# Kernel optimization log

Measured on AMD Instinct MI355X. Metric: run time of the kernel, lower is better.

Reference implementation:

```python
import jax, jax.numpy as jnp
import numpy as np

B, T, C, H = 2, 2048, 1024, 16
DH = C // H


def setup_inputs() -> dict:
    key = jax.random.key(0)
    ks = jax.random.split(key, 5)
    x = jax.random.normal(ks[0], (B, T, C), dtype=jnp.float32)
    qkv_w = jax.random.normal(ks[1], (3 * C, C), dtype=jnp.float32) * (C ** -0.5)
    qkv_b = jnp.zeros((3 * C,), dtype=jnp.float32)
    proj_w = jax.random.normal(ks[2], (C, C), dtype=jnp.float32) * (C ** -0.5)
    proj_b = jnp.zeros((C,), dtype=jnp.float32)
    # init_raw = log(exp(init_decay) - 1) with init_decay = 0.1
    init_raw = float(np.log(np.exp(0.1) - 1.0))
    lambda_raw = jnp.full((H,), init_raw, dtype=jnp.float32)
    return {"x": x, "qkv_w": qkv_w, "qkv_b": qkv_b,
            "proj_w": proj_w, "proj_b": proj_b, "lambda_raw": lambda_raw}


def reference(x, qkv_w, qkv_b, proj_w, proj_b, lambda_raw) -> jnp.ndarray:
    scale = DH ** -0.5
    # qkv projection: [B,T,3C] -> [3,B,H,T,DH]
    qkv = (jnp.einsum('btc,oc->bto', x, qkv_w) + qkv_b)
    qkv = qkv.reshape(B, T, 3, H, DH).transpose(2, 0, 3, 1, 4)
    q, k, v = qkv[0], qkv[1], qkv[2]
    # scores [B,H,T,T]
    attn = jnp.einsum('bhid,bhjd->bhij', q, k) * scale
    # learned per-head exponential decay mask (multiplicative, pre-softmax)
    lambdas = jax.nn.softplus(lambda_raw)  # [H]
    pos = jnp.arange(T, dtype=jnp.float32)
    dist = jnp.abs(pos[:, None] - pos[None, :])  # [T,T]
    decay = jnp.exp(-lambdas[None, :, None, None] * dist[None, None])  # [1,H,T,T]
    attn = jax.nn.softmax(attn * decay, axis=-1)
    out = jnp.einsum('bhij,bhjd->bhid', attn, v)  # [B,H,T,DH]
    out = out.transpose(0, 2, 1, 3).reshape(B, T, C)
    return jnp.einsum('btc,oc->bto', out, proj_w) + proj_b
```

## Files before the change

kernel.cpp:

```cpp
#include <hip/hip_runtime.h>
#include <cstdint>
#include <cstddef>


#define DEVI __device__ __forceinline__

typedef float f32x4 __attribute__((ext_vector_type(4)));
typedef short bf16x8 __attribute__((ext_vector_type(8)));

static constexpr int Bc = 2, Tc = 2048, Cc = 1024, Hc = 16, DHc = 64;

DEVI unsigned short f2bf(float f) {
  union { float f; unsigned u; } a; a.f = f;
  unsigned u = a.u;
  unsigned r = (u + 0x7fffu + ((u >> 16) & 1u)) >> 16;
  return (unsigned short)r;
}

DEVI float bf2f(unsigned short u) {
  union { unsigned u; float f; } a; a.u = ((unsigned)u) << 16;
  return a.f;
}

DEVI unsigned packbf(float lo, float hi) {
  return (unsigned)f2bf(lo) | ((unsigned)f2bf(hi) << 16);
}

DEVI void gload_lds16(const void* g, void* l) {
  __builtin_amdgcn_global_load_lds(
      (const __attribute__((address_space(1))) void*)g,
      (__attribute__((address_space(3))) void*)l, 16, 0, 0);
}

__global__ __launch_bounds__(256) void k_cvt(const float* __restrict__ in,
                                             unsigned short* __restrict__ out,
                                             int n4) {
  int i = blockIdx.x * 256 + threadIdx.x;
  if (i >= n4) return;
  const float4 v = ((const float4*)in)[i];
  ushort4 o;
  o.x = f2bf(v.x); o.y = f2bf(v.y); o.z = f2bf(v.z); o.w = f2bf(v.w);
  ((ushort4*)out)[i] = o;
}

template <int OUT_BF16>
__global__ __launch_bounds__(256) void k_gemm_nt(
    const unsigned short* __restrict__ A, const unsigned short* __restrict__ B,
    const float* __restrict__ bias, void* __restrict__ C, int K, int ldc) {
  __shared__ __align__(16) unsigned short As[128 * 32];
  __shared__ __align__(16) unsigned short Bs[128 * 32];
  const int tid = threadIdx.x, lane = tid & 63, wid = tid >> 6;
  const int wm = wid >> 1, wn = wid & 1;
  const int l15 = lane & 15, l4 = lane >> 4;
  f32x4 acc[4][4] = {};
  const int boff0 = wid * 2048 + lane * 16;
  for (int k0 = 0; k0 < K; k0 += 32) {
    __syncthreads();
#pragma unroll
    for (int s = 0; s < 2; ++s) {
      const int boff = boff0 + s * 1024;
      const int row = boff >> 6, colb = boff & 63;
      gload_lds16((const char*)A + ((size_t)(blockIdx.y * 128 + row) * K + k0) * 2 + colb,
                  (char*)As + (wid * 2 + s) * 1024);
      gload_lds16((const char*)B + ((size_t)(blockIdx.x * 128 + row) * K + k0) * 2 + colb,
                  (char*)Bs + (wid * 2 + s) * 1024);
    }
    __syncthreads();
    bf16x8 af[4], bf[4];
#pragma unroll
    for (int i = 0; i < 4; ++i) {
      af[i] = *(const bf16x8*)(As + (wm * 64 + i * 16 + l15) * 32 + l4 * 8);
      bf[i] = *(const bf16x8*)(Bs + (wn * 64 + i * 16 + l15) * 32 + l4 * 8);
    }
#pragma unroll
    for (int mi = 0; mi < 4; ++mi)
#pragma unroll
      for (int ni = 0; ni < 4; ++ni)
        acc[mi][ni] = __builtin_amdgcn_mfma_f32_16x16x32_bf16(af[mi], bf[ni],
                                                              acc[mi][ni], 0, 0, 0);
  }
#pragma unroll
  for (int mi = 0; mi < 4; ++mi) {
    const int r0 = blockIdx.y * 128 + wm * 64 + mi * 16 + l4 * 4;
#pragma unroll
    for (int ni = 0; ni < 4; ++ni) {
      const int c = blockIdx.x * 128 + wn * 64 + ni * 16 + l15;
      const float bv = bias[c];
#pragma unroll
      for (int j = 0; j < 4; ++j) {
        const float v = acc[mi][ni][j] + bv;
        if (OUT_BF16)
          ((unsigned short*)C)[(size_t)(r0 + j) * ldc + c] = f2bf(v);
        else
          ((float*)C)[(size_t)(r0 + j) * ldc + c] = v;
      }
    }
  }
}

__global__ __launch_bounds__(256) void k_vtrans(const unsigned short* __restrict__ qkv,
                                                unsigned short* __restrict__ vt,
                                                float* __restrict__ vsum) {
  __shared__ unsigned short tile[64][65];
  __shared__ float psum[4][64];
  const int bh = blockIdx.y, b = bh >> 4, h = bh & 15;
  const int t0 = blockIdx.x * 64;
  const int tid = threadIdx.x;
#pragma unroll
  for (int r = 0; r < 16; ++r) {
    const int e = r * 256 + tid;
    const int row = e >> 6, col = e & 63;
    tile[row][col] = qkv[(size_t)(b * Tc + t0 + row) * (3 * Cc) + 2 * Cc + h * DHc + col];
  }
  __syncthreads();
#pragma unroll
  for (int r = 0; r < 16; ++r) {
    const int e = r * 256 + tid;
    const int dd = e >> 6, tcol = e & 63;
    vt[((size_t)bh * DHc + dd) * Tc + t0 + tcol] = tile[tcol][dd];
  }
  const int d = tid & 63, part = tid >> 6;
  float s = 0.f;
#pragma unroll
  for (int k = 0; k < 16; ++k) s += bf2f(tile[part * 16 + k][d]);
  psum[part][d] = s;
  __syncthreads();
  if (tid < 64)
    vsum[((size_t)bh * 32 + blockIdx.x) * 64 + tid] =
        psum[0][tid] + psum[1][tid] + psum[2][tid] + psum[3][tid];
}

__global__ __launch_bounds__(64) void k_prefix(const float* __restrict__ vsum,
                                               float* __restrict__ vpre) {
  const int bh = blockIdx.x, d = threadIdx.x;
  float run = 0.f;
  for (int t = 0; t < 32; ++t) {
    vpre[((size_t)bh * 33 + t) * 64 + d] = run;
    run += vsum[((size_t)bh * 32 + t) * 64 + d];
  }
  vpre[((size_t)bh * 33 + 32) * 64 + d] = run;
}

__global__ __launch_bounds__(256, 2) void k_attn(const unsigned short* __restrict__ qkv,
                                                 const unsigned short* __restrict__ vt,
                                                 const float* __restrict__ lraw,
                                                 const float* __restrict__ vpre,
                                                 unsigned short* __restrict__ ao) {
  __shared__ __align__(16) unsigned short Ks[2][4096];
  __shared__ __align__(16) unsigned short Vs[2][4096];
  const int tid = threadIdx.x, lane = tid & 63, wid = tid >> 6;
  const int l15 = lane & 15, l4 = lane >> 4;
  const int bid = blockIdx.x;
  const int xcd = bid & 7, jj = bid >> 3;
  const int bh = xcd + 8 * (jj >> 4);
  const int qblk = jj & 15;
  const int b = bh >> 4, h = bh & 15;
  const float lam = log1pf(__expf(lraw[h]));
  const int qt0 = qblk * 8 + wid * 2;
  const int qA = qt0 * 16 + l15, qB = qA + 16;

  const int Dstar = (int)fminf(2048.0f, ceilf(18.5f / lam));
  const int q0 = qblk * 128;
  const int t_lo = (q0 > Dstar) ? ((q0 - Dstar) >> 6) : 0;
  const int t_end = min(32, (q0 + Dstar + 191) >> 6);
  const int nfar = 64 * t_lo + (Tc - 64 * t_end);

  const unsigned short* qpA = qkv + (size_t)(b * Tc + qA) * (3 * Cc) + h * DHc + l4 * 8;
  const unsigned short* qpB = qkv + (size_t)(b * Tc + qB) * (3 * Cc) + h * DHc + l4 * 8;
  const bf16x8 qfA0 = *(const bf16x8*)qpA, qfA1 = *(const bf16x8*)(qpA + 32);
  const bf16x8 qfB0 = *(const bf16x8*)qpB, qfB1 = *(const bf16x8*)(qpB + 32);

  const unsigned short* kSrc[2];
  const unsigned short* vSrc[2];
#pragma unroll
  for (int rr = 0; rr < 2; ++rr) {
    const int slot = (rr * 4 + wid) * 64 + lane;
    const int row = slot >> 3, wu = slot & 7;
    kSrc[rr] = qkv + (size_t)(b * Tc + row) * (3 * Cc) + Cc + h * DHc + 8 * (wu ^ (row & 7));
    vSrc[rr] = vt + (size_t)(bh * DHc + row) * Tc + 8 * (wu ^ (row & 7));
  }
  constexpr size_t KTS = (size_t)64 * 3 * Cc;
  int koffs[2][4], voffs[2][4];
#pragma unroll
  for (int hf = 0; hf < 2; ++hf) {
    const int r0 = hf * 32 + l15, r1 = r0 + 16;
    koffs[hf][0] = r0 * 128 + ((l4 ^ (r0 & 7)) * 16);
    koffs[hf][1] = r0 * 128 + (((4 + l4) ^ (r0 & 7)) * 16);
    koffs[hf][2] = r1 * 128 + ((l4 ^ (r1 & 7)) * 16);
    koffs[hf][3] = r1 * 128 + (((4 + l4) ^ (r1 & 7)) * 16);
#pragma unroll
    for (int db = 0; db < 4; ++db) {
      const int rv = db * 16 + l15;
      voffs[hf][db] = rv * 128 + (((hf * 4 + l4) ^ (rv & 7)) * 16);
    }
  }

  const int src0 = l15 | ((l4 & 1) << 5);
  const bool hi = (l4 >= 2);

  f32x4 oA[4], oB[4];
  {
    const float* pre_lo = vpre + ((size_t)bh * 33 + t_lo) * 64;
    const float* pre_hi = vpre + ((size_t)bh * 33 + t_end) * 64;
    const float* pre_all = vpre + ((size_t)bh * 33 + 32) * 64;
#pragma unroll
    for (int di = 0; di < 4; ++di)
#pragma unroll
      for (int j = 0; j < 4; ++j) {
        const int d = di * 16 + l4 * 4 + j;
        const float far = pre_lo[d] + (pre_all[d] - pre_hi[d]);
        oA[di][j] = far;
        oB[di][j] = far;
      }
  }
  float lsumA = 0.f, lsumB = 0.f;

#define STAGE(bb, t)                                                          \
  do {                                                                        \
    _Pragma("unroll") for (int rr = 0; rr < 2; ++rr) {                        \
      gload_lds16(kSrc[rr] + (size_t)(t) * KTS, &Ks[bb][(rr * 4 + wid) * 512]); \
      gload_lds16(vSrc[rr] + (t) * 64, &Vs[bb][(rr * 4 + wid) * 512]);        \
    }                                                                         \
  } while (0)

#define QTILE_P(zz0, zz1, delta_, lsum_, pf_)                                 \
  do {                                                                        \
    float p0[4], p1[4];                                                       \
    _Pragma("unroll") for (int r = 0; r < 4; ++r) {                           \
      const float d0 = 0.125f * __expf(-lam * (float)abs((delta_) - r));      \
      const float d1 = 0.125f * __expf(-lam * (float)abs((delta_) - 16 - r)); \
      p0[r] = __expf(zz0[r] * d0);                                            \
      p1[r] = __expf(zz1[r] * d1);                                            \
      lsum_ += p0[r] + p1[r];                                                 \
    }                                                                         \
    const unsigned pk00 = packbf(p0[0], p0[1]);                               \
    const unsigned pk01 = packbf(p0[2], p0[3]);                               \
    const unsigned pk10 = packbf(p1[0], p1[1]);                               \
    const unsigned pk11 = packbf(p1[2], p1[3]);                               \
    const unsigned a0 = __shfl(pk00, src0, 64), b0 = __shfl(pk10, src0, 64);  \
    const unsigned a1 = __shfl(pk01, src0, 64), b1 = __shfl(pk11, src0, 64);  \
    const unsigned a2 = __shfl(pk00, src0 + 16, 64),                          \
                   b2 = __shfl(pk10, src0 + 16, 64);                          \
    const unsigned a3 = __shfl(pk01, src0 + 16, 64),                          \
                   b3 = __shfl(pk11, src0 + 16, 64);                          \
    pf_.u[0] = hi ? b0 : a0;                                                  \
    pf_.u[1] = hi ? b1 : a1;                                                  \
    pf_.u[2] = hi ? b2 : a2;                                                  \
    pf_.u[3] = hi ? b3 : a3;                                                  \
  } while (0)

#define COMPUTE(bb, kb0)                                                          \
  do {                                                                            \
    const char* kL = (const char*)&Ks[bb][0];                                     \
    const char* vL = (const char*)&Vs[bb][0];                                     \
    _Pragma("unroll") for (int hf = 0; hf < 2; ++hf) {                            \
      const bf16x8 kg0 = *(const bf16x8*)(kL + koffs[hf][0]);                     \
      const bf16x8 kg1 = *(const bf16x8*)(kL + koffs[hf][1]);                     \
      const bf16x8 kg2 = *(const bf16x8*)(kL + koffs[hf][2]);                     \
      const bf16x8 kg3 = *(const bf16x8*)(kL + koffs[hf][3]);                     \
      f32x4 zA0 = {}, zA1 = {}, zB0 = {}, zB1 = {};                               \
      __builtin_amdgcn_s_setprio(1);                                              \
      zA0 = __builtin_amdgcn_mfma_f32_16x16x32_bf16(kg0, qfA0, zA0, 0, 0, 0);     \
      zA0 = __builtin_amdgcn_mfma_f32_16x16x32_bf16(kg1, qfA1, zA0, 0, 0, 0);     \
      zA1 = __builtin_amdgcn_mfma_f32_16x16x32_bf16(kg2, qfA0, zA1, 0, 0, 0);     \
      zA1 = __builtin_amdgcn_mfma_f32_16x16x32_bf16(kg3, qfA1, zA1, 0, 0, 0);     \
      zB0 = __builtin_amdgcn_mfma_f32_16x16x32_bf16(kg0, qfB0, zB0, 0, 0, 0);     \
      zB0 = __builtin_amdgcn_mfma_f32_16x16x32_bf16(kg1, qfB1, zB0, 0, 0, 0);     \
      zB1 = __builtin_amdgcn_mfma_f32_16x16x32_bf16(kg2, qfB0, zB1, 0, 0, 0);     \
      zB1 = __builtin_amdgcn_mfma_f32_16x16x32_bf16(kg3, qfB1, zB1, 0, 0, 0);     \
      __builtin_amdgcn_s_setprio(0);                                              \
      const int dA = qA - (kb0) - hf * 32 - l4 * 4;                               \
      const int dB = dA + 16;                                                     \
      union { unsigned u[4]; bf16x8 v; } pfA, pfB;                                \
      QTILE_P(zA0, zA1, dA, lsumA, pfA);                                          \
      QTILE_P(zB0, zB1, dB, lsumB, pfB);                                          \
      const bf16x8 v0 = *(const bf16x8*)(vL + voffs[hf][0]);                      \
      const bf16x8 v1 = *(const bf16x8*)(vL + voffs[hf][1]);                      \
      const bf16x8 v2 = *(const bf16x8*)(vL + voffs[hf][2]);                      \
      const bf16x8 v3 = *(const bf16x8*)(vL + voffs[hf][3]);                      \
      __builtin_amdgcn_s_setprio(1);                                              \
      oA[0] = __builtin_amdgcn_mfma_f32_16x16x32_bf16(v0, pfA.v, oA[0], 0, 0, 0); \
      oA[1] = __builtin_amdgcn_mfma_f32_16x16x32_bf16(v1, pfA.v, oA[1], 0, 0, 0); \
      oA[2] = __builtin_amdgcn_mfma_f32_16x16x32_bf16(v2, pfA.v, oA[2], 0, 0, 0); \
      oA[3] = __builtin_amdgcn_mfma_f32_16x16x32_bf16(v3, pfA.v, oA[3], 0, 0, 0); \
      oB[0] = __builtin_amdgcn_mfma_f32_16x16x32_bf16(v0, pfB.v, oB[0], 0, 0, 0); \
      oB[1] = __builtin_amdgcn_mfma_f32_16x16x32_bf16(v1, pfB.v, oB[1], 0, 0, 0); \
      oB[2] = __builtin_amdgcn_mfma_f32_16x16x32_bf16(v2, pfB.v, oB[2], 0, 0, 0); \
      oB[3] = __builtin_amdgcn_mfma_f32_16x16x32_bf16(v3, pfB.v, oB[3], 0, 0, 0); \
      __builtin_amdgcn_s_setprio(0);                                              \
    }                                                                             \
  } while (0)

  STAGE(0, t_lo);
  __syncthreads();
  for (int t = t_lo; t < t_end; ++t) {
    const int bb = (t - t_lo) & 1;
    const int tn = (t + 1 < t_end) ? (t + 1) : t_lo;
    STAGE(bb ^ 1, tn);
    COMPUTE(bb, t * 64);
    __syncthreads();
  }
#undef STAGE
#undef QTILE_P
#undef COMPUTE

  lsumA += __shfl_xor(lsumA, 16, 64);
  lsumA += __shfl_xor(lsumA, 32, 64);
  lsumB += __shfl_xor(lsumB, 16, 64);
  lsumB += __shfl_xor(lsumB, 32, 64);
  const float rlA = __builtin_amdgcn_rcpf(lsumA + (float)nfar);
  const float rlB = __builtin_amdgcn_rcpf(lsumB + (float)nfar);

  unsigned short* aopA = ao + (size_t)(b * Tc + qA) * Cc + h * DHc + l4 * 4;
  unsigned short* aopB = ao + (size_t)(b * Tc + qB) * Cc + h * DHc + l4 * 4;
#pragma unroll
  for (int di = 0; di < 4; ++di)
#pragma unroll
    for (int j = 0; j < 4; ++j) {
      aopA[di * 16 + j] = f2bf(oA[di][j] * rlA);
      aopB[di * 16 + j] = f2bf(oB[di][j] * rlB);
    }
}

extern "C" void kernel_launch(void* const* d_in, const int* in_sizes, int n_in,
                              void* d_out, int out_size, void* d_ws, size_t ws_size,
                              hipStream_t stream) {
  const float* x      = (const float*)d_in[0];
  const float* qkv_w  = (const float*)d_in[1];
  const float* qkv_b  = (const float*)d_in[2];
  const float* proj_w = (const float*)d_in[3];
  const float* proj_b = (const float*)d_in[4];
  const float* lraw   = (const float*)d_in[5];

  unsigned short* xb    = (unsigned short*)d_ws;
  unsigned short* wqkv  = xb + 4194304;
  unsigned short* wproj = wqkv + 3145728;
  unsigned short* qkvo  = wproj + 1048576;
  unsigned short* vt    = qkvo + 12582912;
  float*          vsum  = (float*)(vt + 4194304);
  float*          vpre  = vsum + 65536;
  unsigned short* ao    = xb;

  k_cvt<<<4096, 256, 0, stream>>>(x, xb, 1048576);
  k_cvt<<<3072, 256, 0, stream>>>(qkv_w, wqkv, 786432);
  k_cvt<<<1024, 256, 0, stream>>>(proj_w, wproj, 262144);
  k_gemm_nt<1><<<dim3(24, 32), 256, 0, stream>>>(xb, wqkv, qkv_b, qkvo, 1024, 3072);
  k_vtrans<<<dim3(32, 32), 256, 0, stream>>>(qkvo, vt, vsum);
  k_prefix<<<32, 64, 0, stream>>>(vsum, vpre);
  k_attn<<<512, 256, 0, stream>>>(qkvo, vt, lraw, vpre, ao);
  k_gemm_nt<0><<<dim3(8, 32), 256, 0, stream>>>(ao, wproj, proj_b, d_out, 1024, 1024);
}
```

Measured before the change: 187.3 us.

## Replace QKV projection GEMM with 256x256 tiled, LDS-staged, pipelined MFMA kernel

Adds a new GEMM kernel for the QKV projection. It uses 256x256 block tiles with 8 waves, direct global-to-LDS loads with an XOR swizzle, and a double-buffered, phased prefetch schedule using explicit waitcnt, barriers and setprio. It also remaps block indices to improve L2 locality. The aim is more data reuse per tile and overlap of memory loads with MFMA compute. In exchange it uses more LDS and registers, and launches only 192 blocks, which may underfill the GPU.

```diff
diff --git a/kernel.cpp b/kernel.cpp
--- a/kernel.cpp
+++ b/kernel.cpp
@@ -89,6 +89,129 @@
 #pragma unroll
       for (int j = 0; j < 4; ++j) {
         const float v = acc[mi][ni][j] + bv;
+        if (OUT_BF16)
+          ((unsigned short*)C)[(size_t)(r0 + j) * ldc + c] = f2bf(v);
+        else
+          ((float*)C)[(size_t)(r0 + j) * ldc + c] = v;
+      }
+    }
+  }
+}
+
+template <int OUT_BF16>
+__global__ __launch_bounds__(512, 2) void k_gemm256(
+    const unsigned short* __restrict__ A, const unsigned short* __restrict__ B,
+    const float* __restrict__ bias, void* __restrict__ C,
+    int K, int ldc, int NB) {
+  __shared__ __align__(16) unsigned short AS[2][2][8192];
+  __shared__ __align__(16) unsigned short BS[2][2][8192];
+  const int tid = threadIdx.x, lane = tid & 63, wid = tid >> 6;
+  const int wm = wid >> 2, wn = wid & 3;
+  const int l15 = lane & 15, l4 = lane >> 4;
+  const int swz = (blockIdx.x & 7) * (gridDim.x >> 3) + (blockIdx.x >> 3);
+  const int blockM = (swz / NB) * 256, blockN = (swz % NB) * 256;
+
+  const unsigned short* aS[2];
+  const unsigned short* bS[2];
+  char* aD[2]; char* bD[2];
+#pragma unroll
+  for (int g = 0; g < 2; ++g) {
+    const int r = wid * 16 + g * 8 + (lane >> 3);
+    const int cu = ((lane & 7) ^ (r & 7)) * 8;
+    aS[g] = A + (size_t)(blockM + r) * K + cu;
+    bS[g] = B + (size_t)(blockN + r) * K + cu;
+    aD[g] = (char*)&AS[0][0][(wid * 2 + g) * 512];
+    bD[g] = (char*)&BS[0][0][(wid * 2 + g) * 512];
+  }
+  const int T = K >> 6;
+
+#define SG_A(d, h, t)                                                          \
+  do { _Pragma("unroll") for (int g = 0; g < 2; ++g)                           \
+    gload_lds16(aS[g] + (size_t)(h) * 128 * K + (t) * 64,                      \
+                aD[g] + ((d) * 2 + (h)) * 16384); } while (0)
+#define SG_B(d, h, t)                                                          \
+  do { _Pragma("unroll") for (int g = 0; g < 2; ++g)                           \
+    gload_lds16(bS[g] + (size_t)(h) * 128 * K + (t) * 64,                      \
+                bD[g] + ((d) * 2 + (h)) * 16384); } while (0)
+
+  int aoff[4][2], boff[2][2];
+#pragma unroll
+  for (int mt = 0; mt < 4; ++mt)
+#pragma unroll
+    for (int kh = 0; kh < 2; ++kh) {
+      const int r = wm * 64 + mt * 16 + l15;
+      aoff[mt][kh] = r * 128 + (((kh * 4 + l4) ^ (r & 7)) * 16);
+    }
+#pragma unroll
+  for (int nt = 0; nt < 2; ++nt)
+#pragma unroll
+    for (int kh = 0; kh < 2; ++kh) {
+      const int r = wn * 32 + nt * 16 + l15;
+      boff[nt][kh] = r * 128 + (((kh * 4 + l4) ^ (r & 7)) * 16);
+    }
+
+  f32x4 acc[8][4] = {};
+
+  SG_A(0, 0, 0); SG_B(0, 0, 0); SG_A(0, 1, 0); SG_B(0, 1, 0);
+  if (T > 1) {
+    SG_A(1, 0, 1); SG_B(1, 0, 1);
+    asm volatile("s_waitcnt vmcnt(4)" ::: "memory");
+  } else {
+    asm volatile("s_waitcnt vmcnt(0)" ::: "memory");
+  }
+  __builtin_amdgcn_s_barrier();
+  __builtin_amdgcn_sched_barrier(0);
+
+#define PHASE(d, qm, qn, STG, VMODE)                                           \
+  do {                                                                         \
+    const char* aL = (const char*)&AS[d][qm][0];                               \
+    const char* bL = (const char*)&BS[d][qn][0];                               \
+    bf16x8 af[4][2], bfr[2][2];                                                \
+    _Pragma("unroll") for (int mt = 0; mt < 4; ++mt)                           \
+      _Pragma("unroll") for (int kh = 0; kh < 2; ++kh)                         \
+        af[mt][kh] = *(const bf16x8*)(aL + aoff[mt][kh]);                      \
+    _Pragma("unroll") for (int nt = 0; nt < 2; ++nt)                           \
+      _Pragma("unroll") for (int kh = 0; kh < 2; ++kh)                         \
+        bfr[nt][kh] = *(const bf16x8*)(bL + boff[nt][kh]);                     \
+    STG;                                                                       \
+    if ((VMODE) == 1) asm volatile("s_waitcnt vmcnt(4)" ::: "memory");         \
+    if ((VMODE) == 2) asm volatile("s_waitcnt vmcnt(0)" ::: "memory");         \
+    __builtin_amdgcn_s_barrier();                                              \
+    asm volatile("s_waitcnt lgkmcnt(0)" ::: "memory");                         \
+    __builtin_amdgcn_sched_barrier(0);                                         \
+    __builtin_amdgcn_s_setprio(1);                                             \
+    _Pragma("unroll") for (int mt = 0; mt < 4; ++mt)                           \
+      _Pragma("unroll") for (int nt = 0; nt < 2; ++nt) {                       \
+        f32x4& ac = acc[(qm) * 4 + mt][(qn) * 2 + nt];                         \
+        ac = __builtin_amdgcn_mfma_f32_16x16x32_bf16(af[mt][0], bfr[nt][0], ac, 0, 0, 0); \
+        ac = __builtin_amdgcn_mfma_f32_16x16x32_bf16(af[mt][1], bfr[nt][1], ac, 0, 0, 0); \
+      }                                                                        \
+    __builtin_amdgcn_s_setprio(0);                                             \
+    __builtin_amdgcn_s_barrier();                                              \
+    __builtin_amdgcn_sched_barrier(0);                                         \
+  } while (0)
+
+  for (int t = 0; t < T; ++t) {
+    const int d = t & 1;
+    PHASE(d, 0, 0, if (t + 1 < T) SG_A(d ^ 1, 1, t + 1), 0);
+    PHASE(d, 0, 1, if (t + 1 < T) SG_B(d ^ 1, 1, t + 1), 0);
+    PHASE(d, 1, 0, if (t + 2 < T) SG_A(d, 0, t + 2), 0);
+    PHASE(d, 1, 1, if (t + 2 < T) SG_B(d, 0, t + 2), (t + 2 < T) ? 1 : 2);
+  }
+#undef PHASE
+#undef SG_A
+#undef SG_B
+
+#pragma unroll
+  for (int m = 0; m < 8; ++m) {
+    const int r0 = blockM + (m >> 2) * 128 + wm * 64 + (m & 3) * 16 + l4 * 4;
+#pragma unroll
+    for (int n = 0; n < 4; ++n) {
+      const int c = blockN + (n >> 1) * 128 + wn * 32 + (n & 1) * 16 + l15;
+      const float bv = bias[c];
+#pragma unroll
+      for (int j = 0; j < 4; ++j) {
+        const float v = acc[m][n][j] + bv;
         if (OUT_BF16)
           ((unsigned short*)C)[(size_t)(r0 + j) * ldc + c] = f2bf(v);
         else
@@ -344,7 +467,7 @@
   k_cvt<<<4096, 256, 0, stream>>>(x, xb, 1048576);
   k_cvt<<<3072, 256, 0, stream>>>(qkv_w, wqkv, 786432);
   k_cvt<<<1024, 256, 0, stream>>>(proj_w, wproj, 262144);
-  k_gemm_nt<1><<<dim3(24, 32), 256, 0, stream>>>(xb, wqkv, qkv_b, qkvo, 1024, 3072);
+  k_gemm256<1><<<192, 512, 0, stream>>>(xb, wqkv, qkv_b, qkvo, 1024, 3072, 12);
   k_vtrans<<<dim3(32, 32), 256, 0, stream>>>(qkvo, vt, vsum);
   k_prefix<<<32, 64, 0, stream>>>(vsum, vpre);
   k_attn<<<512, 256, 0, stream>>>(qkvo, vt, lraw, vpre, ao);
```

After: 188.5 us. No clear change (+0.6%).

## Double-buffer GEMM LDS tiles with XOR swizzle and block remapping

Applied to the files above, without the earlier changes.

Rewrites the bf16 NT GEMM used for the QKV and output projections. It uses a K-tile of 64 with double-buffered LDS, so the global-to-LDS loads for the next tile are issued while MFMAs run on the current one. It also adds an XOR swizzle on LDS rows to avoid bank conflicts, a 1-D grid with block-index swizzling for L2 locality, and s_setprio around the MFMA blocks. The cost is twice the LDS per block (64KB), which could limit occupancy despite the launch bound of two blocks.

```diff
diff --git a/kernel.cpp b/kernel.cpp
--- a/kernel.cpp
+++ b/kernel.cpp
@@ -44,51 +44,116 @@
 }
 
 template <int OUT_BF16>
-__global__ __launch_bounds__(256) void k_gemm_nt(
+__global__ __launch_bounds__(256, 2) void k_gemm128(
     const unsigned short* __restrict__ A, const unsigned short* __restrict__ B,
-    const float* __restrict__ bias, void* __restrict__ C, int K, int ldc) {
-  __shared__ __align__(16) unsigned short As[128 * 32];
-  __shared__ __align__(16) unsigned short Bs[128 * 32];
+    const float* __restrict__ bias, void* __restrict__ C,
+    int K, int ldc, int NB) {
+  __shared__ __align__(16) unsigned short AS[2][8192];
+  __shared__ __align__(16) unsigned short BS[2][8192];
   const int tid = threadIdx.x, lane = tid & 63, wid = tid >> 6;
   const int wm = wid >> 1, wn = wid & 1;
   const int l15 = lane & 15, l4 = lane >> 4;
+  const int swz = (blockIdx.x & 7) * (gridDim.x >> 3) + (blockIdx.x >> 3);
+  const int blockM = (swz / NB) * 128, blockN = (swz % NB) * 128;
+
+  const unsigned short* aS[4];
+  const unsigned short* bS[4];
+  int ldsOff[4];
+#pragma unroll
+  for (int g = 0; g < 4; ++g) {
+    const int u = g * 256 + tid;
+    const int row = u >> 3;
+    const int wu = (u & 7) ^ (row & 7);
+    aS[g] = A + (size_t)(blockM + row) * K + wu * 8;
+    bS[g] = B + (size_t)(blockN + row) * K + wu * 8;
+    ldsOff[g] = u * 16;
+  }
+  const int T = K >> 6;
+
+#define SG(d, t)                                                               \
+  do {                                                                         \
+    _Pragma("unroll") for (int g = 0; g < 4; ++g) {                            \
+      gload_lds16(aS[g] + (t) * 64, (char*)&AS[d][0] + ldsOff[g]);             \
+      gload_lds16(bS[g] + (t) * 64, (char*)&BS[d][0] + ldsOff[g]);             \
+    }                                                                          \
+  } while (0)
+
+  int aoff[4][2], boff[4][2];
+#pragma unroll
+  for (int mt = 0; mt < 4; ++mt)
+#pragma unroll
+    for (int kh = 0; kh < 2; ++kh) {
+      const int r = wm * 64 + mt * 16 + l15;
+      aoff[mt][kh] = r * 128 + (((kh * 4 + l4) ^ (r & 7)) * 16);
+    }
+#pragma unroll
+  for (int nt = 0; nt < 4; ++nt)
+#pragma unroll
+    for (int kh = 0; kh < 2; ++kh) {
+      const int r = wn * 64 + nt * 16 + l15;
+      boff[nt][kh] = r * 128 + (((kh * 4 + l4) ^ (r & 7)) * 16);
+    }
+
   f32x4 acc[4][4] = {};
-  const int boff0 = wid * 2048 + lane * 16;
-  for (int k0 = 0; k0 < K; k0 += 32) {
-    __syncthreads();
-#pragma unroll
-    for (int s = 0; s < 2; ++s) {
-      const int boff = boff0 + s * 1024;
-      const int row = boff >> 6, colb = boff & 63;
-      gload_lds16((const char*)A + ((size_t)(blockIdx.y * 128 + row) * K + k0) * 2 + colb,
-                  (char*)As + (wid * 2 + s) * 1024);
-      gload_lds16((const char*)B + ((size_t)(blockIdx.x * 128 + row) * K + k0) * 2 + colb,
-                  (char*)Bs + (wid * 2 + s) * 1024);
-    }
-    __syncthreads();
-    bf16x8 af[4], bf[4];
-#pragma unroll
-    for (int i = 0; i < 4; ++i) {
-      af[i] = *(const bf16x8*)(As + (wm * 64 + i * 16 + l15) * 32 + l4 * 8);
-      bf[i] = *(const bf16x8*)(Bs + (wn * 64 + i * 16 + l15) * 32 + l4 * 8);
-    }
-#pragma unroll
-    for (int mi = 0; mi < 4; ++mi)
-#pragma unroll
-      for (int ni = 0; ni < 4; ++ni)
-        acc[mi][ni] = __builtin_amdgcn_mfma_f32_16x16x32_bf16(af[mi], bf[ni],
-                                                              acc[mi][ni], 0, 0, 0);
-  }
-#pragma unroll
-  for (int mi = 0; mi < 4; ++mi) {
-    const int r0 = blockIdx.y * 128 + wm * 64 + mi * 16 + l4 * 4;
-#pragma unroll
-    for (int ni = 0; ni < 4; ++ni) {
-      const int c = blockIdx.x * 128 + wn * 64 + ni * 16 + l15;
+
+  SG(0, 0);
+  asm volatile("s_waitcnt vmcnt(0)" ::: "memory");
+  __builtin_amdgcn_s_barrier();
+  __builtin_amdgcn_sched_barrier(0);
+
+  for (int t = 0; t < T; ++t) {
+    const int d = t & 1;
+    {
+      const char* aL = (const char*)&AS[d][0];
+      const char* bL = (const char*)&BS[d][0];
+      bf16x8 af[4], bf[4];
+#pragma unroll
+      for (int mt = 0; mt < 4; ++mt) af[mt] = *(const bf16x8*)(aL + aoff[mt][0]);
+#pragma unroll
+      for (int nt = 0; nt < 4; ++nt) bf[nt] = *(const bf16x8*)(bL + boff[nt][0]);
+      if (t + 1 < T) SG(d ^ 1, t + 1);
+      __builtin_amdgcn_s_setprio(1);
+#pragma unroll
+      for (int mt = 0; mt < 4; ++mt)
+#pragma unroll
+        for (int nt = 0; nt < 4; ++nt)
+          acc[mt][nt] = __builtin_amdgcn_mfma_f32_16x16x32_bf16(af[mt], bf[nt],
+                                                                acc[mt][nt], 0, 0, 0);
+      __builtin_amdgcn_s_setprio(0);
+    }
+    {
+      const char* aL = (const char*)&AS[d][0];
+      const char* bL = (const char*)&BS[d][0];
+      bf16x8 af[4], bf[4];
+#pragma unroll
+      for (int mt = 0; mt < 4; ++mt) af[mt] = *(const bf16x8*)(aL + aoff[mt][1]);
+#pragma unroll
+      for (int nt = 0; nt < 4; ++nt) bf[nt] = *(const bf16x8*)(bL + boff[nt][1]);
+      asm volatile("s_waitcnt vmcnt(0) lgkmcnt(0)" ::: "memory");
+      __builtin_amdgcn_s_barrier();
+      __builtin_amdgcn_sched_barrier(0);
+      __builtin_amdgcn_s_setprio(1);
+#pragma unroll
+      for (int mt = 0; mt < 4; ++mt)
+#pragma unroll
+        for (int nt = 0; nt < 4; ++nt)
+          acc[mt][nt] = __builtin_amdgcn_mfma_f32_16x16x32_bf16(af[mt], bf[nt],
+                                                                acc[mt][nt], 0, 0, 0);
+      __builtin_amdgcn_s_setprio(0);
+    }
+  }
+#undef SG
+
+#pragma unroll
+  for (int mt = 0; mt < 4; ++mt) {
+    const int r0 = blockM + wm * 64 + mt * 16 + l4 * 4;
+#pragma unroll
+    for (int nt = 0; nt < 4; ++nt) {
+      const int c = blockN + wn * 64 + nt * 16 + l15;
       const float bv = bias[c];
 #pragma unroll
       for (int j = 0; j < 4; ++j) {
-        const float v = acc[mi][ni][j] + bv;
+        const float v = acc[mt][nt][j] + bv;
         if (OUT_BF16)
           ((unsigned short*)C)[(size_t)(r0 + j) * ldc + c] = f2bf(v);
         else
@@ -344,9 +409,9 @@
   k_cvt<<<4096, 256, 0, stream>>>(x, xb, 1048576);
   k_cvt<<<3072, 256, 0, stream>>>(qkv_w, wqkv, 786432);
   k_cvt<<<1024, 256, 0, stream>>>(proj_w, wproj, 262144);
-  k_gemm_nt<1><<<dim3(24, 32), 256, 0, stream>>>(xb, wqkv, qkv_b, qkvo, 1024, 3072);
+  k_gemm128<1><<<768, 256, 0, stream>>>(xb, wqkv, qkv_b, qkvo, 1024, 3072, 24);
   k_vtrans<<<dim3(32, 32), 256, 0, stream>>>(qkvo, vt, vsum);
   k_prefix<<<32, 64, 0, stream>>>(vsum, vpre);
   k_attn<<<512, 256, 0, stream>>>(qkvo, vt, lraw, vpre, ao);
-  k_gemm_nt<0><<<dim3(8, 32), 256, 0, stream>>>(ao, wproj, proj_b, d_out, 1024, 1024);
-}
+  k_gemm128<0><<<256, 256, 0, stream>>>(ao, wproj, proj_b, d_out, 1024, 1024, 8);
+}
```

New measurement: 178.8 us. 1.05x faster.
